# Optimization experiments

Hardware: AMD Instinct MI355X
Metric: run time of the kernel (lower is better)

Reference implementation:

```python
import jax, jax.numpy as jnp
import numpy as np

D_MODEL = 256
D_INNER = 512   # expand=2
D_STATE = 16
D_CONV = 4
DT_RANK = 16    # ceil(d_model/16)
EPS = 1e-5


def _ln(x, g, b):
    m = x.mean(-1, keepdims=True)
    v = jnp.mean((x - m) ** 2, -1, keepdims=True)
    return (x - m) * jax.lax.rsqrt(v + EPS) * g + b


def _mamba(x, W_in, conv_w, conv_b, W_x, W_dt, b_dt, A_log, Dp, W_out):
    B, N, _ = x.shape
    xz = x @ W_in.T                               # [B,N,2*Di]
    xs, z = jnp.split(xz, 2, axis=-1)
    # depthwise causal conv1d, kernel D_CONV, left pad D_CONV-1
    xp = jnp.pad(xs, ((0, 0), (D_CONV - 1, 0), (0, 0)))
    xc = sum(xp[:, k:k + N, :] * conv_w[:, k] for k in range(D_CONV)) + conv_b
    xc = jax.nn.silu(xc)                          # [B,N,Di]
    dbl = xc @ W_x.T                              # [B,N,dt_rank+2*S]
    dt, Bm, Cm = jnp.split(dbl, [DT_RANK, DT_RANK + D_STATE], axis=-1)
    dt = jax.nn.softplus(dt @ W_dt.T + b_dt)      # [B,N,Di]
    A = -jnp.exp(A_log)                           # [Di,S]
    dA = jnp.exp(dt[..., None] * A)               # [B,N,Di,S]
    dBx = dt[..., None] * Bm[:, :, None, :] * xc[..., None]

    def step(h, inp):
        dA_t, dBx_t, c_t = inp                    # [B,Di,S],[B,Di,S],[B,S]
        h = dA_t * h + dBx_t
        y = jnp.einsum('bds,bs->bd', h, c_t)
        return h, y

    h0 = jnp.zeros((B, D_INNER, D_STATE), xs.dtype)
    _, ys = jax.lax.scan(step, h0, (dA.swapaxes(0, 1), dBx.swapaxes(0, 1), Cm.swapaxes(0, 1)))
    y = ys.swapaxes(0, 1) + Dp * xc
    y = y * jax.nn.silu(z)
    return y @ W_out.T                            # [B,N,d_model]


def setup_inputs() -> dict:
    key = jax.random.key(0)
    ks = jax.random.split(key, 24)
    g = lambda k, s, sc=0.02: jax.random.normal(k, s, jnp.float32) * sc
    inp = {}
    inp['input_states'] = jax.random.normal(ks[0], (1, 8192, D_MODEL), jnp.float32)
    inp['position_states'] = jax.random.normal(ks[1], (1, 8192, D_MODEL), jnp.float32)
    inp['W_in'] = g(ks[2], (2 * D_INNER, D_MODEL))
    inp['conv_w'] = g(ks[3], (D_INNER, D_CONV), 0.2)
    inp['conv_b'] = jnp.zeros((D_INNER,), jnp.float32)
    inp['W_x'] = g(ks[4], (DT_RANK + 2 * D_STATE, D_INNER))
    inp['W_dt'] = g(ks[5], (D_INNER, DT_RANK), 0.1)
    inp['b_dt'] = g(ks[6], (D_INNER,), 0.1)
    # S4D-real init: A_log = log(1..d_state) broadcast over channels
    inp['A_log'] = jnp.log(jnp.broadcast_to(jnp.arange(1, D_STATE + 1, dtype=jnp.float32), (D_INNER, D_STATE)))
    inp['Dp'] = jnp.ones((D_INNER,), jnp.float32)
    inp['W_out'] = g(ks[7], (D_MODEL, D_INNER))
    inp['W_lin'] = g(ks[8], (D_MODEL, D_MODEL))
    inp['b_lin'] = jnp.zeros((D_MODEL,), jnp.float32)
    inp['ln1_g'] = jnp.ones((D_MODEL,), jnp.float32)
    inp['ln1_b'] = jnp.zeros((D_MODEL,), jnp.float32)
    inp['W_exp'] = g(ks[9], (2 * D_MODEL, D_MODEL))
    inp['b_exp'] = jnp.zeros((2 * D_MODEL,), jnp.float32)
    inp['W_sq'] = g(ks[10], (D_MODEL, 2 * D_MODEL))
    inp['b_sq'] = jnp.zeros((D_MODEL,), jnp.float32)
    inp['ln2_g'] = jnp.ones((D_MODEL,), jnp.float32)
    inp['ln2_b'] = jnp.zeros((D_MODEL,), jnp.float32)
    return inp


def reference(input_states, position_states, W_in, conv_w, conv_b, W_x, W_dt, b_dt,
              A_log, Dp, W_out, W_lin, b_lin, ln1_g, ln1_b, W_exp, b_exp, W_sq, b_sq,
              ln2_g, ln2_b):
    h = _mamba(input_states, W_in, conv_w, conv_b, W_x, W_dt, b_dt, A_log, Dp, W_out)
    h = h @ W_lin.T + b_lin
    h = _ln(h + input_states, ln1_g, ln1_b)
    ff = jax.nn.relu(h @ W_exp.T + b_exp) @ W_sq.T + b_sq
    out = _ln(h + ff, ln2_g, ln2_b)
    # RPEMamba returns (hidden, input_states) as (states, attention_scores)
    return out, input_states
```

## Files before the change

kernel.cpp:

```cpp
#include <hip/hip_runtime.h>
#include <stdint.h>

#define NT 8192
#define DM 256
#define DI 512
#define DS 16
#define DR 16
#define NCH 512
#define LCH 16
#define NSUP 32
#define CPS 16

typedef __bf16 bf16_t;
typedef bf16_t bf16x8 __attribute__((ext_vector_type(8)));
typedef float f32x4 __attribute__((ext_vector_type(4)));

__device__ __forceinline__ unsigned short f2b(float f) {
    union { float f; unsigned int i; } v; v.f = f;
    unsigned int r = v.i + 0x7fffu + ((v.i >> 16) & 1u);
    return (unsigned short)(r >> 16);
}
__device__ __forceinline__ float b2f(unsigned short u) {
    union { unsigned int i; float f; } v; v.i = ((unsigned int)u) << 16; return v.f;
}
__device__ __forceinline__ bf16x8 ld_frag_lds(const unsigned short* p) {
    union { uint4 u; bf16x8 b; } v;
    v.u = *(const uint4*)p;
    return v.b;
}
__device__ __forceinline__ void async16(const unsigned short* g, unsigned short* l) {
    __builtin_amdgcn_global_load_lds(
        (const __attribute__((address_space(1))) unsigned int*)g,
        (__attribute__((address_space(3))) unsigned int*)l, 16, 0, 0);
}
__device__ __forceinline__ float fast_softplus(float x) {
    return x > 20.f ? x : __logf(1.f + __expf(x));
}
__device__ __forceinline__ float silu(float x) {
    return x / (1.f + __expf(-x));
}

struct CvtArgs {
    const float* src[7];
    unsigned short* dst[7];
    int cnt[7];
    int total;
};
__global__ __launch_bounds__(256) void cvt_all(CvtArgs a) {
    int i = blockIdx.x * 256 + threadIdx.x;
    if (i >= a.total) return;
    #pragma unroll
    for (int s = 0; s < 7; s++) {
        if (i < a.cnt[s]) {
            unsigned short v = f2b(a.src[s][i]);
            if (s == 3) {
                int k = i >> 9, j = i & 511;
                a.dst[s][j * 256 + k] = v;
            } else {
                a.dst[s][i] = v;
            }
            return;
        }
        i -= a.cnt[s];
    }
}

template<int BM, int BN, int FLAGS>
__global__ __launch_bounds__(256) void gemm_lds(
    const unsigned short* __restrict__ A, const unsigned short* __restrict__ B,
    int M, int N, int K,
    const float* __restrict__ bias, const float* __restrict__ resid,
    float* __restrict__ Cf, unsigned short* __restrict__ Cb)
{
    constexpr int MI = BM / 32;
    constexpr int NJ = BN / 32;
    __shared__ unsigned short sA[BM * 64];
    __shared__ unsigned short sB[BN * 64];
    const int tid = threadIdx.x;
    const int m0 = blockIdx.x * BM;
    const int n0 = blockIdx.y * BN;
    const int wave = tid >> 6, lane = tid & 63;
    const int wm = (wave & 1) * (BM / 2);
    const int wn = (wave >> 1) * (BN / 2);
    const int qm = lane >> 4, rm = lane & 15;

    f32x4 acc[MI][NJ];
    #pragma unroll
    for (int i = 0; i < MI; i++)
        #pragma unroll
        for (int j = 0; j < NJ; j++)
            #pragma unroll
            for (int r = 0; r < 4; r++) acc[i][j][r] = 0.f;

    const int sr = tid >> 3;
    const int sc = (tid & 7) * 8;

    for (int k0 = 0; k0 < K; k0 += 64) {
        __syncthreads();
        #pragma unroll
        for (int j = 0; j < BM / 32; j++) {
            int r = sr + j * 32;
            async16(A + (size_t)(m0 + r) * K + k0 + sc, &sA[r * 64 + sc]);
        }
        #pragma unroll
        for (int j = 0; j < BN / 32; j++) {
            int r = sr + j * 32;
            if (n0 + r < N)
                async16(B + (size_t)(n0 + r) * K + k0 + sc, &sB[r * 64 + sc]);
        }
        __syncthreads();
        #pragma unroll
        for (int ks = 0; ks < 64; ks += 32) {
            bf16x8 af[MI], bfr[NJ];
            #pragma unroll
            for (int i = 0; i < MI; i++)
                af[i] = ld_frag_lds(&sA[(wm + i * 16 + rm) * 64 + ks + qm * 8]);
            #pragma unroll
            for (int j = 0; j < NJ; j++)
                bfr[j] = ld_frag_lds(&sB[(wn + j * 16 + rm) * 64 + ks + qm * 8]);
            #pragma unroll
            for (int i = 0; i < MI; i++)
                #pragma unroll
                for (int j = 0; j < NJ; j++)
                    acc[i][j] = __builtin_amdgcn_mfma_f32_16x16x32_bf16(
                        af[i], bfr[j], acc[i][j], 0, 0, 0);
        }
    }

    #pragma unroll
    for (int i = 0; i < MI; i++) {
        int mrow = m0 + wm + i * 16 + qm * 4;
        #pragma unroll
        for (int j = 0; j < NJ; j++) {
            int ncol = n0 + wn + j * 16 + rm;
            if (ncol < N) {
                #pragma unroll
                for (int r = 0; r < 4; r++) {
                    float v = acc[i][j][r];
                    int mm = mrow + r;
                    if constexpr (FLAGS & 1) v += bias[ncol];
                    if constexpr (FLAGS & 4) v += resid[(size_t)mm * N + ncol];
                    if constexpr (FLAGS & 2) v = v > 0.f ? v : 0.f;
                    if constexpr (FLAGS & 8) Cf[(size_t)mm * N + ncol] = v;
                    if constexpr (FLAGS & 16) Cb[(size_t)mm * N + ncol] = f2b(v);
                }
            }
        }
    }
}

__global__ __launch_bounds__(256) void conv_silu_b(
    const unsigned short* __restrict__ xz, const float* __restrict__ cw,
    const float* __restrict__ cb, unsigned short* __restrict__ xcb)
{
    int idx = blockIdx.x * 256 + threadIdx.x;
    int d = idx & (DI - 1), t = idx >> 9;
    float v = cb[d];
    #pragma unroll
    for (int k = 0; k < 4; k++) {
        int tt = t - 3 + k;
        if (tt >= 0) v += b2f(xz[(size_t)tt * 1024 + d]) * cw[d * 4 + k];
    }
    xcb[idx] = f2b(silu(v));
}

__global__ __launch_bounds__(256, 4) void scan1(
    const unsigned short* __restrict__ xz, const float* __restrict__ cw,
    const float* __restrict__ cbp, const float* __restrict__ dbl,
    const float* __restrict__ Wdt, const float* __restrict__ bdt,
    const float* __restrict__ A_log,
    float* __restrict__ Ac, float* __restrict__ Bc)
{
    __shared__ float sR[LCH * 48];
    const int d = blockIdx.x * 256 + threadIdx.x;
    const int c = blockIdx.y;
    const int t0 = c * LCH;
    {
        const float4* src = (const float4*)(dbl + (size_t)t0 * 48);
        if (threadIdx.x < 192) ((float4*)sR)[threadIdx.x] = src[threadIdx.x];
    }
    __syncthreads();
    const float cw0 = cw[d*4], cw1 = cw[d*4+1], cw2 = cw[d*4+2], cw3 = cw[d*4+3];
    const float cb = cbp[d];
    const unsigned short* xzp = xz + d;
    float x0 = (t0 >= 3) ? b2f(xzp[(size_t)(t0-3) * 1024]) : 0.f;
    float x1 = (t0 >= 2) ? b2f(xzp[(size_t)(t0-2) * 1024]) : 0.f;
    float x2 = (t0 >= 1) ? b2f(xzp[(size_t)(t0-1) * 1024]) : 0.f;
    float w[DR], A[DS], h[DS];
    #pragma unroll
    for (int j = 0; j < DR; j++) w[j] = Wdt[d * DR + j];
    const float bd = bdt[d];
    #pragma unroll
    for (int s = 0; s < DS; s++) { A[s] = -__expf(A_log[d * DS + s]); h[s] = 0.f; }
    float sumdt = 0.f;
    #pragma unroll 4
    for (int t = 0; t < LCH; t++) {
        float x3 = b2f(xzp[(size_t)(t0 + t) * 1024]);
        float cv = cb + x0 * cw0 + x1 * cw1 + x2 * cw2 + x3 * cw3;
        x0 = x1; x1 = x2; x2 = x3;
        float xcv = silu(cv);
        const float* r = &sR[t * 48];
        float4 rd[4], rb[4];
        #pragma unroll
        for (int k = 0; k < 4; k++) { rd[k] = ((const float4*)r)[k]; rb[k] = ((const float4*)r)[4 + k]; }
        float accd = bd;
        #pragma unroll
        for (int k = 0; k < 4; k++)
            accd += rd[k].x * w[4*k] + rd[k].y * w[4*k+1] + rd[k].z * w[4*k+2] + rd[k].w * w[4*k+3];
        float dtv = fast_softplus(accd);
        sumdt += dtv;
        float dtx = dtv * xcv;
        const float* bptr = (const float*)rb;
        #pragma unroll
        for (int s = 0; s < DS; s++)
            h[s] = __expf(dtv * A[s]) * h[s] + dtx * bptr[s];
    }
    #pragma unroll
    for (int s = 0; s < DS; s++) {
        size_t off = ((size_t)c * DS + s) * DI + d;
        Ac[off] = __expf(sumdt * A[s]);
        Bc[off] = h[s];
    }
}

__global__ __launch_bounds__(256) void scan2a(
    const float* __restrict__ Ac, const float* __restrict__ Bc,
    float* __restrict__ Ap, float* __restrict__ Hl,
    float* __restrict__ Es, float* __restrict__ Ds)
{
    int p = blockIdx.x * 256 + threadIdx.x;
    int j = blockIdx.y;
    float h = 0.f, P = 1.f;
    for (int cc = 0; cc < CPS; cc++) {
        size_t off = (size_t)(j * CPS + cc) * 8192 + p;
        Hl[off] = h; Ap[off] = P;
        float a = Ac[off];
        h = a * h + Bc[off];
        P *= a;
    }
    Es[(size_t)j * 8192 + p] = h;
    Ds[(size_t)j * 8192 + p] = P;
}

__global__ __launch_bounds__(256) void scan2b(
    const float* __restrict__ Es, const float* __restrict__ Ds,
    float* __restrict__ Ss)
{
    int p = blockIdx.x * 256 + threadIdx.x;
    float S = 0.f;
    for (int j = 0; j < NSUP; j++) {
        Ss[(size_t)j * 8192 + p] = S;
        S = Ds[(size_t)j * 8192 + p] * S + Es[(size_t)j * 8192 + p];
    }
}

__global__ __launch_bounds__(256, 4) void scan3(
    const unsigned short* __restrict__ xz, const float* __restrict__ cw,
    const float* __restrict__ cbp, const float* __restrict__ dbl,
    const float* __restrict__ Wdt, const float* __restrict__ bdt,
    const float* __restrict__ A_log, const float* __restrict__ Dpp,
    const float* __restrict__ Ap, const float* __restrict__ Hl,
    const float* __restrict__ Ss, unsigned short* __restrict__ ygb)
{
    __shared__ float sR[LCH * 48];
    const int d = blockIdx.x * 256 + threadIdx.x;
    const int c = blockIdx.y;
    const int jsup = c / CPS;
    const int t0 = c * LCH;
    {
        const float4* src = (const float4*)(dbl + (size_t)t0 * 48);
        if (threadIdx.x < 192) ((float4*)sR)[threadIdx.x] = src[threadIdx.x];
    }
    __syncthreads();
    const float cw0 = cw[d*4], cw1 = cw[d*4+1], cw2 = cw[d*4+2], cw3 = cw[d*4+3];
    const float cb = cbp[d];
    const unsigned short* xzp = xz + d;
    const unsigned short* zp  = xz + DI + d;
    float x0 = (t0 >= 3) ? b2f(xzp[(size_t)(t0-3) * 1024]) : 0.f;
    float x1 = (t0 >= 2) ? b2f(xzp[(size_t)(t0-2) * 1024]) : 0.f;
    float x2 = (t0 >= 1) ? b2f(xzp[(size_t)(t0-1) * 1024]) : 0.f;
    float w[DR], A[DS], h[DS];
    #pragma unroll
    for (int j = 0; j < DR; j++) w[j] = Wdt[d * DR + j];
    const float bd = bdt[d];
    const float dpv = Dpp[d];
    #pragma unroll
    for (int s = 0; s < DS; s++) {
        A[s] = -__expf(A_log[d * DS + s]);
        size_t off = (size_t)c * 8192 + s * DI + d;
        h[s] = Ap[off] * Ss[(size_t)jsup * 8192 + s * DI + d] + Hl[off];
    }
    #pragma unroll 4
    for (int t = 0; t < LCH; t++) {
        float x3 = b2f(xzp[(size_t)(t0 + t) * 1024]);
        float zv = b2f(zp[(size_t)(t0 + t) * 1024]);
        float cv = cb + x0 * cw0 + x1 * cw1 + x2 * cw2 + x3 * cw3;
        x0 = x1; x1 = x2; x2 = x3;
        float xcv = silu(cv);
        const float* r = &sR[t * 48];
        float4 rd[4], rb[4], rc[4];
        #pragma unroll
        for (int k = 0; k < 4; k++) {
            rd[k] = ((const float4*)r)[k];
            rb[k] = ((const float4*)r)[4 + k];
            rc[k] = ((const float4*)r)[8 + k];
        }
        float accd = bd;
        #pragma unroll
        for (int k = 0; k < 4; k++)
            accd += rd[k].x * w[4*k] + rd[k].y * w[4*k+1] + rd[k].z * w[4*k+2] + rd[k].w * w[4*k+3];
        float dtv = fast_softplus(accd);
        float dtx = dtv * xcv;
        const float* bptr = (const float*)rb;
        const float* cptr = (const float*)rc;
        float y = 0.f;
        #pragma unroll
        for (int s = 0; s < DS; s++) {
            h[s] = __expf(dtv * A[s]) * h[s] + dtx * bptr[s];
            y += h[s] * cptr[s];
        }
        ygb[(size_t)(t0 + t) * DI + d] = f2b((y + dpv * xcv) * silu(zv));
    }
}

__global__ __launch_bounds__(256) void lnorm(
    const float* __restrict__ X, const float* __restrict__ X2,
    const float* __restrict__ g, const float* __restrict__ b,
    float* __restrict__ outf, unsigned short* __restrict__ outb,
    const float* __restrict__ csrc, float* __restrict__ cdst)
{
    int wave = threadIdx.x >> 6, lane = threadIdx.x & 63;
    int row = blockIdx.x * 4 + wave;
    const float* x = X + (size_t)row * DM;
    float v[4];
    #pragma unroll
    for (int i = 0; i < 4; i++) {
        int col = lane + i * 64;
        v[i] = x[col];
        if (X2) v[i] += X2[(size_t)row * DM + col];
    }
    if (cdst) {
        #pragma unroll
        for (int i = 0; i < 4; i++) {
            int col = lane + i * 64;
            cdst[(size_t)row * DM + col] = csrc[(size_t)row * DM + col];
        }
    }
    float s = v[0] + v[1] + v[2] + v[3];
    float s2 = v[0]*v[0] + v[1]*v[1] + v[2]*v[2] + v[3]*v[3];
    #pragma unroll
    for (int m = 1; m < 64; m <<= 1) {
        s  += __shfl_xor(s, m, 64);
        s2 += __shfl_xor(s2, m, 64);
    }
    float mean = s * (1.f / DM);
    float var = s2 * (1.f / DM) - mean * mean;
    float inv = rsqrtf(var + 1e-5f);
    #pragma unroll
    for (int i = 0; i < 4; i++) {
        int col = lane + i * 64;
        float o = (v[i] - mean) * inv * g[col] + b[col];
        if (outf) outf[(size_t)row * DM + col] = o;
        if (outb) outb[(size_t)row * DM + col] = f2b(o);
    }
}

static constexpr size_t OFF_XZB   = 0;
static constexpr size_t OFF_XCB   = 16777216;
static constexpr size_t OFF_DBL   = 25165824;
static constexpr size_t OFF_AC    = 26738688;
static constexpr size_t OFF_BC    = 43515904;
static constexpr size_t OFF_HL    = 60293120;
static constexpr size_t OFF_AP    = 77070336;
static constexpr size_t OFF_ES    = 93847552;
static constexpr size_t OFF_DS2   = 94896128;
static constexpr size_t OFF_SS    = 95944704;
static constexpr size_t OFF_YGB   = 96993280;
static constexpr size_t OFF_XB    = 105381888;
static constexpr size_t OFF_WINB  = 109576192;
static constexpr size_t OFF_WXB   = 110100480;
static constexpr size_t OFF_WOUTT = 110149632;
static constexpr size_t OFF_WLINB = 110411776;
static constexpr size_t OFF_WEXPB = 110542848;
static constexpr size_t OFF_WSQB  = 110804992;
static constexpr size_t OFF_WCOMB = 111067136;
static constexpr size_t OFF_H2    = OFF_AC;
static constexpr size_t OFF_HLN   = OFF_BC;
static constexpr size_t OFF_HLNB  = OFF_BC + 8388608;
static constexpr size_t OFF_FF1B  = OFF_HL;
static constexpr size_t OFF_FF2   = OFF_AP;

extern "C" void kernel_launch(void* const* d_in, const int* in_sizes, int n_in,
                              void* d_out, int out_size, void* d_ws, size_t ws_size,
                              hipStream_t stream)
{
    const float* x      = (const float*)d_in[0];
    const float* W_in   = (const float*)d_in[2];
    const float* conv_w = (const float*)d_in[3];
    const float* conv_b = (const float*)d_in[4];
    const float* W_x    = (const float*)d_in[5];
    const float* W_dt   = (const float*)d_in[6];
    const float* b_dt   = (const float*)d_in[7];
    const float* A_log  = (const float*)d_in[8];
    const float* Dp     = (const float*)d_in[9];
    const float* W_out  = (const float*)d_in[10];
    const float* W_lin  = (const float*)d_in[11];
    const float* b_lin  = (const float*)d_in[12];
    const float* ln1_g  = (const float*)d_in[13];
    const float* ln1_b  = (const float*)d_in[14];
    const float* W_exp  = (const float*)d_in[15];
    const float* b_exp  = (const float*)d_in[16];
    const float* W_sq   = (const float*)d_in[17];
    const float* b_sq   = (const float*)d_in[18];
    const float* ln2_g  = (const float*)d_in[19];
    const float* ln2_b  = (const float*)d_in[20];

    char* ws = (char*)d_ws;
    unsigned short* xzb = (unsigned short*)(ws + OFF_XZB);
    unsigned short* xcb = (unsigned short*)(ws + OFF_XCB);
    float* dbl  = (float*)(ws + OFF_DBL);
    float* Ac   = (float*)(ws + OFF_AC);
    float* Bc   = (float*)(ws + OFF_BC);
    float* Hl   = (float*)(ws + OFF_HL);
    float* Ap   = (float*)(ws + OFF_AP);
    float* Es   = (float*)(ws + OFF_ES);
    float* Ds   = (float*)(ws + OFF_DS2);
    float* Ss   = (float*)(ws + OFF_SS);
    unsigned short* ygb   = (unsigned short*)(ws + OFF_YGB);
    unsigned short* xb    = (unsigned short*)(ws + OFF_XB);
    unsigned short* winb  = (unsigned short*)(ws + OFF_WINB);
    unsigned short* wxb   = (unsigned short*)(ws + OFF_WXB);
    unsigned short* woutT = (unsigned short*)(ws + OFF_WOUTT);
    unsigned short* wlinb = (unsigned short*)(ws + OFF_WLINB);
    unsigned short* wexpb = (unsigned short*)(ws + OFF_WEXPB);
    unsigned short* wsqb  = (unsigned short*)(ws + OFF_WSQB);
    unsigned short* wcomb = (unsigned short*)(ws + OFF_WCOMB);
    float* h2   = (float*)(ws + OFF_H2);
    float* hln  = (float*)(ws + OFF_HLN);
    unsigned short* hlnb  = (unsigned short*)(ws + OFF_HLNB);
    unsigned short* ff1b  = (unsigned short*)(ws + OFF_FF1B);
    float* ff2  = (float*)(ws + OFF_FF2);
    float* outp = (float*)d_out;

    CvtArgs ca;
    ca.src[0] = x;     ca.dst[0] = xb;    ca.cnt[0] = NT * DM;
    ca.src[1] = W_in;  ca.dst[1] = winb;  ca.cnt[1] = 1024 * DM;
    ca.src[2] = W_x;   ca.dst[2] = wxb;   ca.cnt[2] = 48 * DI;
    ca.src[3] = W_out; ca.dst[3] = woutT; ca.cnt[3] = DM * DI;
    ca.src[4] = W_lin; ca.dst[4] = wlinb; ca.cnt[4] = DM * DM;
    ca.src[5] = W_exp; ca.dst[5] = wexpb; ca.cnt[5] = DI * DM;
    ca.src[6] = W_sq;  ca.dst[6] = wsqb;  ca.cnt[6] = DM * DI;
    ca.total = ca.cnt[0]+ca.cnt[1]+ca.cnt[2]+ca.cnt[3]+ca.cnt[4]+ca.cnt[5]+ca.cnt[6];
    cvt_all<<<(ca.total + 255) / 256, 256, 0, stream>>>(ca);

    gemm_lds<64,64,16><<<dim3(4, 8), 256, 0, stream>>>(wlinb, woutT, DM, DI, DM,
                                                       nullptr, nullptr, nullptr, wcomb);
    gemm_lds<128,128,16><<<dim3(64, 8), 256, 0, stream>>>(xb, winb, NT, 1024, DM,
                                                          nullptr, nullptr, nullptr, xzb);
    conv_silu_b<<<NT * DI / 256, 256, 0, stream>>>(xzb, conv_w, conv_b, xcb);
    gemm_lds<64,64,8><<<dim3(128, 1), 256, 0, stream>>>(xcb, wxb, NT, 48, DI,
                                                        nullptr, nullptr, dbl, nullptr);
    scan1<<<dim3(2, NCH), 256, 0, stream>>>(xzb, conv_w, conv_b, dbl, W_dt, b_dt,
                                            A_log, Ac, Bc);
    scan2a<<<dim3(32, NSUP), 256, 0, stream>>>(Ac, Bc, Ap, Hl, Es, Ds);
    scan2b<<<32, 256, 0, stream>>>(Es, Ds, Ss);
    scan3<<<dim3(2, NCH), 256, 0, stream>>>(xzb, conv_w, conv_b, dbl, W_dt, b_dt,
                                            A_log, Dp, Ap, Hl, Ss, ygb);
    gemm_lds<64,64,1|4|8><<<dim3(128, 4), 256, 0, stream>>>(ygb, wcomb, NT, DM, DI,
                                                            b_lin, x, h2, nullptr);
    lnorm<<<NT / 4, 256, 0, stream>>>(h2, nullptr, ln1_g, ln1_b, hln, hlnb,
                                      nullptr, nullptr);
    gemm_lds<64,128,1|2|16><<<dim3(128, 4), 256, 0, stream>>>(hlnb, wexpb, NT, DI, DM,
                                                              b_exp, nullptr, nullptr, ff1b);
    gemm_lds<64,64,1|8><<<dim3(128, 4), 256, 0, stream>>>(ff1b, wsqb, NT, DM, DI,
                                                          b_sq, nullptr, ff2, nullptr);
    lnorm<<<NT / 4, 256, 0, stream>>>(hln, ff2, ln2_g, ln2_b, outp, nullptr,
                                      x, outp + (size_t)NT * DM);
}
```

Before: 286.1 us.

## Fold dt projection into x_proj GEMM, split scan state across lanes, bf16 chunk states

Precomputes a combined weight W_dt·W_x[:16] and appends the B/C rows, so one GEMM over xc produces softplus(dt) directly as a full fp32 [N,512] tensor plus the B/C columns. The scan kernels stop recomputing conv, silu and the dt projection and read dt and xc from memory instead. Each channel's 16 states are split across two lanes, combined with a shuffle, to raise parallelism. Intermediate chunk state buffers are stored in bf16 to cut memory traffic. In exchange, a 16 MB dt tensor is written and read twice, and the bf16 chunk states lose precision.

```diff
diff --git a/kernel.cpp b/kernel.cpp
--- a/kernel.cpp
+++ b/kernel.cpp
@@ -40,28 +40,44 @@
     return x / (1.f + __expf(-x));
 }
 
-struct CvtArgs {
-    const float* src[7];
-    unsigned short* dst[7];
-    int cnt[7];
-    int total;
+struct PrepArgs {
+    const float* src[6];
+    unsigned short* dst[6];
+    int cnt[6];
+    int cvt_blocks;
+    const float* W_dt;
+    const float* W_x;
+    unsigned short* wbig;
 };
-__global__ __launch_bounds__(256) void cvt_all(CvtArgs a) {
-    int i = blockIdx.x * 256 + threadIdx.x;
-    if (i >= a.total) return;
-    #pragma unroll
-    for (int s = 0; s < 7; s++) {
-        if (i < a.cnt[s]) {
-            unsigned short v = f2b(a.src[s][i]);
-            if (s == 3) {
-                int k = i >> 9, j = i & 511;
-                a.dst[s][j * 256 + k] = v;
-            } else {
-                a.dst[s][i] = v;
+__global__ __launch_bounds__(256) void prep(PrepArgs a) {
+    int blk = blockIdx.x;
+    if (blk < a.cvt_blocks) {
+        int i = blk * 256 + threadIdx.x;
+        #pragma unroll
+        for (int s = 0; s < 6; s++) {
+            if (i < a.cnt[s]) {
+                unsigned short v = f2b(a.src[s][i]);
+                if (s == 2) {
+                    int k = i >> 9, j = i & 511;
+                    a.dst[s][j * 256 + k] = v;
+                } else {
+                    a.dst[s][i] = v;
+                }
+                return;
             }
-            return;
-        }
-        i -= a.cnt[s];
+            i -= a.cnt[s];
+        }
+    } else if (blk < a.cvt_blocks + 1024) {
+        int i = (blk - a.cvt_blocks) * 256 + threadIdx.x;
+        int d = i >> 9, k = i & 511;
+        float acc = 0.f;
+        #pragma unroll
+        for (int j = 0; j < 16; j++) acc += a.W_dt[d * 16 + j] * a.W_x[j * 512 + k];
+        a.wbig[d * 512 + k] = f2b(acc);
+    } else {
+        int i = (blk - a.cvt_blocks - 1024) * 256 + threadIdx.x;
+        int j = i >> 9, k = i & 511;
+        a.wbig[(512 + j) * 512 + k] = f2b(a.W_x[(16 + j) * 512 + k]);
     }
 }
 
@@ -70,7 +86,8 @@
     const unsigned short* __restrict__ A, const unsigned short* __restrict__ B,
     int M, int N, int K,
     const float* __restrict__ bias, const float* __restrict__ resid,
-    float* __restrict__ Cf, unsigned short* __restrict__ Cb)
+    float* __restrict__ Cf, unsigned short* __restrict__ Cb,
+    float* __restrict__ Cf2)
 {
     constexpr int MI = BM / 32;
     constexpr int NJ = BN / 32;
@@ -138,11 +155,20 @@
                 for (int r = 0; r < 4; r++) {
                     float v = acc[i][j][r];
                     int mm = mrow + r;
-                    if constexpr (FLAGS & 1) v += bias[ncol];
-                    if constexpr (FLAGS & 4) v += resid[(size_t)mm * N + ncol];
-                    if constexpr (FLAGS & 2) v = v > 0.f ? v : 0.f;
-                    if constexpr (FLAGS & 8) Cf[(size_t)mm * N + ncol] = v;
-                    if constexpr (FLAGS & 16) Cb[(size_t)mm * N + ncol] = f2b(v);
+                    if constexpr (FLAGS & 32) {
+                        if (ncol < 512) {
+                            v = fast_softplus(v + bias[ncol]);
+                            Cf[(size_t)mm * 512 + ncol] = v;
+                        } else {
+                            Cf2[(size_t)mm * 32 + (ncol - 512)] = v;
+                        }
+                    } else {
+                        if constexpr (FLAGS & 1) v += bias[ncol];
+                        if constexpr (FLAGS & 4) v += resid[(size_t)mm * N + ncol];
+                        if constexpr (FLAGS & 2) v = v > 0.f ? v : 0.f;
+                        if constexpr (FLAGS & 8) Cf[(size_t)mm * N + ncol] = v;
+                        if constexpr (FLAGS & 16) Cb[(size_t)mm * N + ncol] = f2b(v);
+                    }
                 }
             }
         }
@@ -164,68 +190,51 @@
     xcb[idx] = f2b(silu(v));
 }
 
-__global__ __launch_bounds__(256, 4) void scan1(
-    const unsigned short* __restrict__ xz, const float* __restrict__ cw,
-    const float* __restrict__ cbp, const float* __restrict__ dbl,
-    const float* __restrict__ Wdt, const float* __restrict__ bdt,
-    const float* __restrict__ A_log,
-    float* __restrict__ Ac, float* __restrict__ Bc)
-{
-    __shared__ float sR[LCH * 48];
-    const int d = blockIdx.x * 256 + threadIdx.x;
+__global__ __launch_bounds__(256) void scan1(
+    const unsigned short* __restrict__ xcb, const float* __restrict__ dtf,
+    const float* __restrict__ dblf, const float* __restrict__ A_log,
+    unsigned short* __restrict__ Acb, unsigned short* __restrict__ Bcb)
+{
+    __shared__ float sBC[LCH * 32];
+    const int tid = threadIdx.x;
+    const int d = blockIdx.x * 128 + (tid >> 1);
+    const int sd = tid & 1;
     const int c = blockIdx.y;
     const int t0 = c * LCH;
-    {
-        const float4* src = (const float4*)(dbl + (size_t)t0 * 48);
-        if (threadIdx.x < 192) ((float4*)sR)[threadIdx.x] = src[threadIdx.x];
-    }
+    if (tid < 128)
+        ((float4*)sBC)[tid] = ((const float4*)(dblf + (size_t)t0 * 32))[tid];
     __syncthreads();
-    const float cw0 = cw[d*4], cw1 = cw[d*4+1], cw2 = cw[d*4+2], cw3 = cw[d*4+3];
-    const float cb = cbp[d];
-    const unsigned short* xzp = xz + d;
-    float x0 = (t0 >= 3) ? b2f(xzp[(size_t)(t0-3) * 1024]) : 0.f;
-    float x1 = (t0 >= 2) ? b2f(xzp[(size_t)(t0-2) * 1024]) : 0.f;
-    float x2 = (t0 >= 1) ? b2f(xzp[(size_t)(t0-1) * 1024]) : 0.f;
-    float w[DR], A[DS], h[DS];
-    #pragma unroll
-    for (int j = 0; j < DR; j++) w[j] = Wdt[d * DR + j];
-    const float bd = bdt[d];
-    #pragma unroll
-    for (int s = 0; s < DS; s++) { A[s] = -__expf(A_log[d * DS + s]); h[s] = 0.f; }
+    float A2[8], h[8];
+    #pragma unroll
+    for (int s = 0; s < 8; s++) {
+        A2[s] = -__expf(A_log[d * 16 + sd * 8 + s]) * 1.44269504f;
+        h[s] = 0.f;
+    }
     float sumdt = 0.f;
     #pragma unroll 4
     for (int t = 0; t < LCH; t++) {
-        float x3 = b2f(xzp[(size_t)(t0 + t) * 1024]);
-        float cv = cb + x0 * cw0 + x1 * cw1 + x2 * cw2 + x3 * cw3;
-        x0 = x1; x1 = x2; x2 = x3;
-        float xcv = silu(cv);
-        const float* r = &sR[t * 48];
-        float4 rd[4], rb[4];
-        #pragma unroll
-        for (int k = 0; k < 4; k++) { rd[k] = ((const float4*)r)[k]; rb[k] = ((const float4*)r)[4 + k]; }
-        float accd = bd;
-        #pragma unroll
-        for (int k = 0; k < 4; k++)
-            accd += rd[k].x * w[4*k] + rd[k].y * w[4*k+1] + rd[k].z * w[4*k+2] + rd[k].w * w[4*k+3];
-        float dtv = fast_softplus(accd);
+        float dtv = dtf[(size_t)(t0 + t) * DI + d];
+        float xcv = b2f(xcb[(size_t)(t0 + t) * DI + d]);
+        float dtx = dtv * xcv;
         sumdt += dtv;
-        float dtx = dtv * xcv;
-        const float* bptr = (const float*)rb;
-        #pragma unroll
-        for (int s = 0; s < DS; s++)
-            h[s] = __expf(dtv * A[s]) * h[s] + dtx * bptr[s];
-    }
-    #pragma unroll
-    for (int s = 0; s < DS; s++) {
-        size_t off = ((size_t)c * DS + s) * DI + d;
-        Ac[off] = __expf(sumdt * A[s]);
-        Bc[off] = h[s];
+        const float4 b0 = *(const float4*)&sBC[t * 32 + sd * 8];
+        const float4 b1 = *(const float4*)&sBC[t * 32 + sd * 8 + 4];
+        float bb[8] = {b0.x, b0.y, b0.z, b0.w, b1.x, b1.y, b1.z, b1.w};
+        #pragma unroll
+        for (int s = 0; s < 8; s++)
+            h[s] = exp2f(dtv * A2[s]) * h[s] + dtx * bb[s];
+    }
+    #pragma unroll
+    for (int s = 0; s < 8; s++) {
+        size_t off = ((size_t)c * DS + sd * 8 + s) * DI + d;
+        Acb[off] = f2b(exp2f(sumdt * A2[s]));
+        Bcb[off] = f2b(h[s]);
     }
 }
 
 __global__ __launch_bounds__(256) void scan2a(
-    const float* __restrict__ Ac, const float* __restrict__ Bc,
-    float* __restrict__ Ap, float* __restrict__ Hl,
+    const unsigned short* __restrict__ Acb, const unsigned short* __restrict__ Bcb,
+    unsigned short* __restrict__ Apb, unsigned short* __restrict__ Hlb,
     float* __restrict__ Es, float* __restrict__ Ds)
 {
     int p = blockIdx.x * 256 + threadIdx.x;
@@ -233,10 +242,9 @@
     float h = 0.f, P = 1.f;
     for (int cc = 0; cc < CPS; cc++) {
         size_t off = (size_t)(j * CPS + cc) * 8192 + p;
-        Hl[off] = h; Ap[off] = P;
-        float a = Ac[off];
-        h = a * h + Bc[off];
-        P *= a;
+        Hlb[off] = f2b(h); Apb[off] = f2b(P);
+        h = b2f(Acb[off]) * h + b2f(Bcb[off]);
+        P *= b2f(Acb[off]);
     }
     Es[(size_t)j * 8192 + p] = h;
     Ds[(size_t)j * 8192 + p] = P;
@@ -254,72 +262,53 @@
     }
 }
 
-__global__ __launch_bounds__(256, 4) void scan3(
-    const unsigned short* __restrict__ xz, const float* __restrict__ cw,
-    const float* __restrict__ cbp, const float* __restrict__ dbl,
-    const float* __restrict__ Wdt, const float* __restrict__ bdt,
+__global__ __launch_bounds__(256) void scan3(
+    const unsigned short* __restrict__ xcb, const float* __restrict__ dtf,
+    const float* __restrict__ dblf, const unsigned short* __restrict__ xzb,
     const float* __restrict__ A_log, const float* __restrict__ Dpp,
-    const float* __restrict__ Ap, const float* __restrict__ Hl,
+    const unsigned short* __restrict__ Apb, const unsigned short* __restrict__ Hlb,
     const float* __restrict__ Ss, unsigned short* __restrict__ ygb)
 {
-    __shared__ float sR[LCH * 48];
-    const int d = blockIdx.x * 256 + threadIdx.x;
+    __shared__ float sBC[LCH * 32];
+    const int tid = threadIdx.x;
+    const int d = blockIdx.x * 128 + (tid >> 1);
+    const int sd = tid & 1;
     const int c = blockIdx.y;
     const int jsup = c / CPS;
     const int t0 = c * LCH;
-    {
-        const float4* src = (const float4*)(dbl + (size_t)t0 * 48);
-        if (threadIdx.x < 192) ((float4*)sR)[threadIdx.x] = src[threadIdx.x];
-    }
+    if (tid < 128)
+        ((float4*)sBC)[tid] = ((const float4*)(dblf + (size_t)t0 * 32))[tid];
     __syncthreads();
-    const float cw0 = cw[d*4], cw1 = cw[d*4+1], cw2 = cw[d*4+2], cw3 = cw[d*4+3];
-    const float cb = cbp[d];
-    const unsigned short* xzp = xz + d;
-    const unsigned short* zp  = xz + DI + d;
-    float x0 = (t0 >= 3) ? b2f(xzp[(size_t)(t0-3) * 1024]) : 0.f;
-    float x1 = (t0 >= 2) ? b2f(xzp[(size_t)(t0-2) * 1024]) : 0.f;
-    float x2 = (t0 >= 1) ? b2f(xzp[(size_t)(t0-1) * 1024]) : 0.f;
-    float w[DR], A[DS], h[DS];
-    #pragma unroll
-    for (int j = 0; j < DR; j++) w[j] = Wdt[d * DR + j];
-    const float bd = bdt[d];
+    float A2[8], h[8];
+    #pragma unroll
+    for (int s = 0; s < 8; s++) {
+        A2[s] = -__expf(A_log[d * 16 + sd * 8 + s]) * 1.44269504f;
+        size_t off = (size_t)c * 8192 + (sd * 8 + s) * DI + d;
+        h[s] = b2f(Apb[off]) * Ss[(size_t)jsup * 8192 + (sd * 8 + s) * DI + d]
+             + b2f(Hlb[off]);
+    }
     const float dpv = Dpp[d];
-    #pragma unroll
-    for (int s = 0; s < DS; s++) {
-        A[s] = -__expf(A_log[d * DS + s]);
-        size_t off = (size_t)c * 8192 + s * DI + d;
-        h[s] = Ap[off] * Ss[(size_t)jsup * 8192 + s * DI + d] + Hl[off];
-    }
     #pragma unroll 4
     for (int t = 0; t < LCH; t++) {
-        float x3 = b2f(xzp[(size_t)(t0 + t) * 1024]);
-        float zv = b2f(zp[(size_t)(t0 + t) * 1024]);
-        float cv = cb + x0 * cw0 + x1 * cw1 + x2 * cw2 + x3 * cw3;
-        x0 = x1; x1 = x2; x2 = x3;
-        float xcv = silu(cv);
-        const float* r = &sR[t * 48];
-        float4 rd[4], rb[4], rc[4];
-        #pragma unroll
-        for (int k = 0; k < 4; k++) {
-            rd[k] = ((const float4*)r)[k];
-            rb[k] = ((const float4*)r)[4 + k];
-            rc[k] = ((const float4*)r)[8 + k];
-        }
-        float accd = bd;
-        #pragma unroll
-        for (int k = 0; k < 4; k++)
-            accd += rd[k].x * w[4*k] + rd[k].y * w[4*k+1] + rd[k].z * w[4*k+2] + rd[k].w * w[4*k+3];
-        float dtv = fast_softplus(accd);
+        float dtv = dtf[(size_t)(t0 + t) * DI + d];
+        float xcv = b2f(xcb[(size_t)(t0 + t) * DI + d]);
+        float zv  = b2f(xzb[(size_t)(t0 + t) * 1024 + DI + d]);
         float dtx = dtv * xcv;
-        const float* bptr = (const float*)rb;
-        const float* cptr = (const float*)rc;
+        const float4 b0 = *(const float4*)&sBC[t * 32 + sd * 8];
+        const float4 b1 = *(const float4*)&sBC[t * 32 + sd * 8 + 4];
+        const float4 c0 = *(const float4*)&sBC[t * 32 + 16 + sd * 8];
+        const float4 c1 = *(const float4*)&sBC[t * 32 + 16 + sd * 8 + 4];
+        float bb[8] = {b0.x, b0.y, b0.z, b0.w, b1.x, b1.y, b1.z, b1.w};
+        float cc[8] = {c0.x, c0.y, c0.z, c0.w, c1.x, c1.y, c1.z, c1.w};
         float y = 0.f;
         #pragma unroll
-        for (int s = 0; s < DS; s++) {
-            h[s] = __expf(dtv * A[s]) * h[s] + dtx * bptr[s];
-            y += h[s] * cptr[s];
-        }
-        ygb[(size_t)(t0 + t) * DI + d] = f2b((y + dpv * xcv) * silu(zv));
+        for (int s = 0; s < 8; s++) {
+            h[s] = exp2f(dtv * A2[s]) * h[s] + dtx * bb[s];
+            y += h[s] * cc[s];
+        }
+        y += __shfl_xor(y, 1, 64);
+        if (!sd)
+            ygb[(size_t)(t0 + t) * DI + d] = f2b((y + dpv * xcv) * silu(zv));
     }
 }
 
@@ -367,28 +356,29 @@
 
 static constexpr size_t OFF_XZB   = 0;
 static constexpr size_t OFF_XCB   = 16777216;
-static constexpr size_t OFF_DBL   = 25165824;
-static constexpr size_t OFF_AC    = 26738688;
-static constexpr size_t OFF_BC    = 43515904;
-static constexpr size_t OFF_HL    = 60293120;
-static constexpr size_t OFF_AP    = 77070336;
-static constexpr size_t OFF_ES    = 93847552;
-static constexpr size_t OFF_DS2   = 94896128;
-static constexpr size_t OFF_SS    = 95944704;
-static constexpr size_t OFF_YGB   = 96993280;
-static constexpr size_t OFF_XB    = 105381888;
-static constexpr size_t OFF_WINB  = 109576192;
-static constexpr size_t OFF_WXB   = 110100480;
-static constexpr size_t OFF_WOUTT = 110149632;
-static constexpr size_t OFF_WLINB = 110411776;
-static constexpr size_t OFF_WEXPB = 110542848;
-static constexpr size_t OFF_WSQB  = 110804992;
-static constexpr size_t OFF_WCOMB = 111067136;
-static constexpr size_t OFF_H2    = OFF_AC;
-static constexpr size_t OFF_HLN   = OFF_BC;
-static constexpr size_t OFF_HLNB  = OFF_BC + 8388608;
-static constexpr size_t OFF_FF1B  = OFF_HL;
-static constexpr size_t OFF_FF2   = OFF_AP;
+static constexpr size_t OFF_DTF   = 25165824;
+static constexpr size_t OFF_DBLF  = 41943040;
+static constexpr size_t OFF_ACB   = 42991616;
+static constexpr size_t OFF_BCB   = 51380224;
+static constexpr size_t OFF_APB   = 59768832;
+static constexpr size_t OFF_HLB   = 68157440;
+static constexpr size_t OFF_ES    = 76546048;
+static constexpr size_t OFF_DS2   = 77594624;
+static constexpr size_t OFF_SS    = 78643200;
+static constexpr size_t OFF_YGB   = 79691776;
+static constexpr size_t OFF_XB    = 88080384;
+static constexpr size_t OFF_WINB  = 92274688;
+static constexpr size_t OFF_WOUTT = 92798976;
+static constexpr size_t OFF_WLINB = 93061120;
+static constexpr size_t OFF_WEXPB = 93192192;
+static constexpr size_t OFF_WSQB  = 93454336;
+static constexpr size_t OFF_WCOMB = 93716480;
+static constexpr size_t OFF_WBIG  = 93978624;
+static constexpr size_t OFF_H2    = 94535680;
+static constexpr size_t OFF_HLN   = 102924288;
+static constexpr size_t OFF_HLNB  = 111312896;
+static constexpr size_t OFF_FF1B  = 115507200;
+static constexpr size_t OFF_FF2   = 123895808;
 
 extern "C" void kernel_launch(void* const* d_in, const int* in_sizes, int n_in,
                               void* d_out, int out_size, void* d_ws, size_t ws_size,
@@ -418,23 +408,24 @@
     char* ws = (char*)d_ws;
     unsigned short* xzb = (unsigned short*)(ws + OFF_XZB);
     unsigned short* xcb = (unsigned short*)(ws + OFF_XCB);
-    float* dbl  = (float*)(ws + OFF_DBL);
-    float* Ac   = (float*)(ws + OFF_AC);
-    float* Bc   = (float*)(ws + OFF_BC);
-    float* Hl   = (float*)(ws + OFF_HL);
-    float* Ap   = (float*)(ws + OFF_AP);
+    float* dtf  = (float*)(ws + OFF_DTF);
+    float* dblf = (float*)(ws + OFF_DBLF);
+    unsigned short* Acb = (unsigned short*)(ws + OFF_ACB);
+    unsigned short* Bcb = (unsigned short*)(ws + OFF_BCB);
+    unsigned short* Apb = (unsigned short*)(ws + OFF_APB);
+    unsigned short* Hlb = (unsigned short*)(ws + OFF_HLB);
     float* Es   = (float*)(ws + OFF_ES);
     float* Ds   = (float*)(ws + OFF_DS2);
     float* Ss   = (float*)(ws + OFF_SS);
     unsigned short* ygb   = (unsigned short*)(ws + OFF_YGB);
     unsigned short* xb    = (unsigned short*)(ws + OFF_XB);
     unsigned short* winb  = (unsigned short*)(ws + OFF_WINB);
-    unsigned short* wxb   = (unsigned short*)(ws + OFF_WXB);
     unsigned short* woutT = (unsigned short*)(ws + OFF_WOUTT);
     unsigned short* wlinb = (unsigned short*)(ws + OFF_WLINB);
     unsigned short* wexpb = (unsigned short*)(ws + OFF_WEXPB);
     unsigned short* wsqb  = (unsigned short*)(ws + OFF_WSQB);
     unsigned short* wcomb = (unsigned short*)(ws + OFF_WCOMB);
+    unsigned short* wbig  = (unsigned short*)(ws + OFF_WBIG);
     float* h2   = (float*)(ws + OFF_H2);
     float* hln  = (float*)(ws + OFF_HLN);
     unsigned short* hlnb  = (unsigned short*)(ws + OFF_HLNB);
@@ -442,38 +433,37 @@
     float* ff2  = (float*)(ws + OFF_FF2);
     float* outp = (float*)d_out;
 
-    CvtArgs ca;
-    ca.src[0] = x;     ca.dst[0] = xb;    ca.cnt[0] = NT * DM;
-    ca.src[1] = W_in;  ca.dst[1] = winb;  ca.cnt[1] = 1024 * DM;
-    ca.src[2] = W_x;   ca.dst[2] = wxb;   ca.cnt[2] = 48 * DI;
-    ca.src[3] = W_out; ca.dst[3] = woutT; ca.cnt[3] = DM * DI;
-    ca.src[4] = W_lin; ca.dst[4] = wlinb; ca.cnt[4] = DM * DM;
-    ca.src[5] = W_exp; ca.dst[5] = wexpb; ca.cnt[5] = DI * DM;
-    ca.src[6] = W_sq;  ca.dst[6] = wsqb;  ca.cnt[6] = DM * DI;
-    ca.total = ca.cnt[0]+ca.cnt[1]+ca.cnt[2]+ca.cnt[3]+ca.cnt[4]+ca.cnt[5]+ca.cnt[6];
-    cvt_all<<<(ca.total + 255) / 256, 256, 0, stream>>>(ca);
+    PrepArgs pa;
+    pa.src[0] = x;     pa.dst[0] = xb;    pa.cnt[0] = NT * DM;
+    pa.src[1] = W_in;  pa.dst[1] = winb;  pa.cnt[1] = 1024 * DM;
+    pa.src[2] = W_out; pa.dst[2] = woutT; pa.cnt[2] = DM * DI;
+    pa.src[3] = W_lin; pa.dst[3] = wlinb; pa.cnt[3] = DM * DM;
+    pa.src[4] = W_exp; pa.dst[4] = wexpb; pa.cnt[4] = DI * DM;
+    pa.src[5] = W_sq;  pa.dst[5] = wsqb;  pa.cnt[5] = DM * DI;
+    pa.cvt_blocks = (2097152 + 262144 + 131072 + 65536 + 131072 + 131072) / 256;
+    pa.W_dt = W_dt; pa.W_x = W_x; pa.wbig = wbig;
+    prep<<<pa.cvt_blocks + 1024 + 64, 256, 0, stream>>>(pa);
 
     gemm_lds<64,64,16><<<dim3(4, 8), 256, 0, stream>>>(wlinb, woutT, DM, DI, DM,
-                                                       nullptr, nullptr, nullptr, wcomb);
+        nullptr, nullptr, nullptr, wcomb, nullptr);
     gemm_lds<128,128,16><<<dim3(64, 8), 256, 0, stream>>>(xb, winb, NT, 1024, DM,
-                                                          nullptr, nullptr, nullptr, xzb);
+        nullptr, nullptr, nullptr, xzb, nullptr);
     conv_silu_b<<<NT * DI / 256, 256, 0, stream>>>(xzb, conv_w, conv_b, xcb);
-    gemm_lds<64,64,8><<<dim3(128, 1), 256, 0, stream>>>(xcb, wxb, NT, 48, DI,
-                                                        nullptr, nullptr, dbl, nullptr);
-    scan1<<<dim3(2, NCH), 256, 0, stream>>>(xzb, conv_w, conv_b, dbl, W_dt, b_dt,
-                                            A_log, Ac, Bc);
-    scan2a<<<dim3(32, NSUP), 256, 0, stream>>>(Ac, Bc, Ap, Hl, Es, Ds);
+    gemm_lds<64,64,32><<<dim3(128, 9), 256, 0, stream>>>(xcb, wbig, NT, 544, DI,
+        b_dt, nullptr, dtf, nullptr, dblf);
+    scan1<<<dim3(4, NCH), 256, 0, stream>>>(xcb, dtf, dblf, A_log, Acb, Bcb);
+    scan2a<<<dim3(32, NSUP), 256, 0, stream>>>(Acb, Bcb, Apb, Hlb, Es, Ds);
     scan2b<<<32, 256, 0, stream>>>(Es, Ds, Ss);
-    scan3<<<dim3(2, NCH), 256, 0, stream>>>(xzb, conv_w, conv_b, dbl, W_dt, b_dt,
-                                            A_log, Dp, Ap, Hl, Ss, ygb);
+    scan3<<<dim3(4, NCH), 256, 0, stream>>>(xcb, dtf, dblf, xzb, A_log, Dp,
+                                            Apb, Hlb, Ss, ygb);
     gemm_lds<64,64,1|4|8><<<dim3(128, 4), 256, 0, stream>>>(ygb, wcomb, NT, DM, DI,
-                                                            b_lin, x, h2, nullptr);
+        b_lin, x, h2, nullptr, nullptr);
     lnorm<<<NT / 4, 256, 0, stream>>>(h2, nullptr, ln1_g, ln1_b, hln, hlnb,
                                       nullptr, nullptr);
     gemm_lds<64,128,1|2|16><<<dim3(128, 4), 256, 0, stream>>>(hlnb, wexpb, NT, DI, DM,
-                                                              b_exp, nullptr, nullptr, ff1b);
+        b_exp, nullptr, nullptr, ff1b, nullptr);
     gemm_lds<64,64,1|8><<<dim3(128, 4), 256, 0, stream>>>(ff1b, wsqb, NT, DM, DI,
-                                                          b_sq, nullptr, ff2, nullptr);
+        b_sq, nullptr, ff2, nullptr, nullptr);
     lnorm<<<NT / 4, 256, 0, stream>>>(hln, ff2, ln2_g, ln2_b, outp, nullptr,
                                       x, outp + (size_t)NT * DM);
 }
```

After: 279.1 us. 1.02x faster.
